# Kernel optimization log

Measured on AMD Instinct MI355X. Metric: run time of the kernel, lower is better.

## Reference

```python
import jax, jax.numpy as jnp
import numpy as np

EPS = 1e-5


def _mamba(x, in_w, conv_w, conv_b, x_w, dt_w, dt_b, A_log, D, out_w):
    # x: [B, L, d_model] -> [B, L, d_model]; mamba_ssm defaults (bias-free in/out proj)
    Bsz, L, _ = x.shape
    d_inner, d_conv = conv_w.shape
    dt_rank = dt_w.shape[1]
    N = A_log.shape[1]

    xz = x @ in_w.T                              # [B, L, 2*d_inner]
    u, z = jnp.split(xz, 2, axis=-1)

    # causal depthwise conv (torch pads both sides by d_conv-1 then slices [:L])
    uc = jnp.pad(u.transpose(0, 2, 1), ((0, 0), (0, 0), (d_conv - 1, 0)))  # [B, d, L+pad]
    uc = jax.lax.conv_general_dilated(
        uc, conv_w[:, None, :], window_strides=(1,), padding='VALID',
        feature_group_count=d_inner, dimension_numbers=('NCH', 'OIH', 'NCH'))
    u = jax.nn.silu(uc + conv_b[None, :, None]).transpose(0, 2, 1)          # [B, L, d]

    xdbc = u @ x_w.T                              # [B, L, dt_rank + 2N]
    dt, Bm, Cm = jnp.split(xdbc, [dt_rank, dt_rank + N], axis=-1)
    delta = jax.nn.softplus(dt @ dt_w.T + dt_b)   # [B, L, d]

    A = -jnp.exp(A_log)                           # [d, N]
    dA = jnp.exp(delta[..., None] * A)            # [B, L, d, N]
    dBu = delta[..., None] * Bm[:, :, None, :] * u[..., None]  # [B, L, d, N]

    def step(h, inp):
        dA_t, dBu_t, C_t = inp
        h = dA_t * h + dBu_t                      # [B, d, N]
        y = jnp.einsum('bdn,bn->bd', h, C_t)
        return h, y

    h0 = jnp.zeros((Bsz, d_inner, N), dA.dtype)
    _, ys = jax.lax.scan(step, h0,
                         (dA.transpose(1, 0, 2, 3), dBu.transpose(1, 0, 2, 3), Cm.transpose(1, 0, 2)))
    y = ys.transpose(1, 0, 2)                     # [B, L, d]
    y = (y + u * D) * jax.nn.silu(z)
    return y @ out_w.T


def reference(x, input_lengths, m, emb, conv_w, conv_b, ln_g, ln_b,
              f_in_w, f_conv_w, f_conv_b, f_x_w, f_dt_w, f_dt_b, f_A_log, f_D, f_out_w,
              b_in_w, b_conv_w, b_conv_b, b_x_w, b_dt_w, b_dt_b, b_A_log, b_D, b_out_w,
              proj_w, proj_b):
    K = conv_w.shape[-1]
    pad = (K - 1) // 2
    h = emb[x].transpose(0, 2, 1)                 # [B, C, L]
    for i in range(conv_w.shape[0]):
        h = jax.lax.conv_general_dilated(h, conv_w[i], (1,), [(pad, pad)],
                                         dimension_numbers=('NCH', 'OIH', 'NCH'))
        h = h + conv_b[i][None, :, None]
        mu = h.mean(axis=1, keepdims=True)
        var = ((h - mu) ** 2).mean(axis=1, keepdims=True)
        h = (h - mu) * jax.lax.rsqrt(var + EPS)
        h = h * ln_g[i][None, :, None] + ln_b[i][None, :, None]
        h = jnp.where(h > 0, h, 0.2 * h)          # LeakyReLU(0.2); dropout is eval no-op
        h = jnp.where(m[:, None, :], 0.0, h)
    h = h.transpose(0, 2, 1)                      # [B, L, C]
    fo = _mamba(h, f_in_w, f_conv_w, f_conv_b, f_x_w, f_dt_w, f_dt_b, f_A_log, f_D, f_out_w)
    bo = _mamba(h[:, ::-1], b_in_w, b_conv_w, b_conv_b, b_x_w, b_dt_w, b_dt_b, b_A_log, b_D, b_out_w)
    comb = jnp.concatenate([fo, bo], axis=-1) @ proj_w.T + proj_b
    return jnp.where(m[:, :, None], 0.0, comb)


def setup_inputs() -> dict:
    key = jax.random.key(0)
    ks = iter(jax.random.split(key, 40))
    B, L, C, K, depth, V = 4, 1024, 512, 5, 3, 178
    d_inner, d_state, d_conv, dt_rank = 2 * C, 16, 4, 32
    inp = {
        'x': jax.random.randint(next(ks), (B, L), 0, V),
        'input_lengths': jax.random.randint(next(ks), (B,), 1, L + 1),
        'm': jnp.zeros((B, L), dtype=bool),
        'emb': jax.random.normal(next(ks), (V, C)),
        'conv_w': jax.random.normal(next(ks), (depth, C, C, K)) * 0.05,
        'conv_b': jax.random.normal(next(ks), (depth, C)) * 0.05,
        'ln_g': jnp.ones((depth, C)),
        'ln_b': jnp.zeros((depth, C)),
        'proj_w': jax.random.normal(next(ks), (C, 2 * C)) * 0.02,
        'proj_b': jax.random.normal(next(ks), (C,)) * 0.02,
    }
    for p in ('f', 'b'):
        inp[p + '_in_w'] = jax.random.normal(next(ks), (2 * d_inner, C)) * 0.02
        inp[p + '_conv_w'] = jax.random.normal(next(ks), (d_inner, d_conv)) * 0.1
        inp[p + '_conv_b'] = jax.random.normal(next(ks), (d_inner,)) * 0.1
        inp[p + '_x_w'] = jax.random.normal(next(ks), (dt_rank + 2 * d_state, d_inner)) * 0.02
        inp[p + '_dt_w'] = jax.random.normal(next(ks), (d_inner, dt_rank)) * 0.02
        inp[p + '_dt_b'] = jax.random.normal(next(ks), (d_inner,)) * 0.1
        inp[p + '_A_log'] = jax.random.uniform(next(ks), (d_inner, d_state))
        inp[p + '_D'] = jax.random.normal(next(ks), (d_inner,)) * 0.1
        inp[p + '_out_w'] = jax.random.normal(next(ks), (C, d_inner)) * 0.02
    return inp
```

## Files before the change

### kernel.cpp

```cpp
#include <hip/hip_runtime.h>
#include <hip/hip_bf16.h>

typedef __attribute__((ext_vector_type(8))) short short8;
typedef __attribute__((ext_vector_type(4))) float f32x4;
typedef __attribute__((ext_vector_type(4))) unsigned short ushort4_t;

#define BSZ 4
#define LSEQ 1024
#define CCH 512
#define BL (BSZ*LSEQ)
#define BL2 (2*BL)
#define DI 1024
#define NST 16
#define DTR 32
#define NCH 32
#define CLEN 32

__device__ __forceinline__ float sigmoidf_(float x){ return 1.f/(1.f+__expf(-x)); }
__device__ __forceinline__ float softplus_(float x){ return x > 20.f ? x : log1pf(__expf(x)); }
__device__ __forceinline__ unsigned short f2bf_(float f){
  __hip_bfloat16 h = __float2bfloat16(f); return *(unsigned short*)&h;
}

typedef const __attribute__((address_space(1))) unsigned int* gas_t;
typedef __attribute__((address_space(3))) unsigned int* las_t;
__device__ __forceinline__ void gload16(const void* g, void* l){
  __builtin_amdgcn_global_load_lds((gas_t)g, (las_t)l, 16, 0, 0);
}


struct CastEnt { const float* s; unsigned short* d; unsigned n4, acc; };
struct CastArgs { CastEnt e[9]; unsigned total4; };
__global__ void k_cast_all(CastArgs a){
  unsigned i = blockIdx.x*256 + threadIdx.x;
  if (i >= a.total4) return;
  #pragma unroll
  for (int k=0;k<9;k++){
    if (i < a.e[k].acc + a.e[k].n4){
      unsigned j = i - a.e[k].acc;
      float4 v = ((const float4*)a.e[k].s)[j];
      ushort4_t o = { f2bf_(v.x), f2bf_(v.y), f2bf_(v.z), f2bf_(v.w) };
      *(ushort4_t*)(a.e[k].d + (size_t)j*4) = o;
      return;
    }
  }
}

__global__ void k_prep_convw(const float* __restrict__ cw, __hip_bfloat16* __restrict__ wt){
  int i = blockIdx.x*256 + threadIdx.x;
  const int total = 3*CCH*CCH*5;
  if (i >= total) return;
  int j = i % (CCH*5);
  int co = (i/(CCH*5)) % CCH;
  int layer = i/(CCH*5*CCH);
  int k = j >> 9, ci = j & 511;
  wt[i] = __float2bfloat16(cw[(((size_t)layer*CCH + co)*CCH + ci)*5 + k]);
}

__global__ void k_embed(const int* __restrict__ x, const float* __restrict__ emb,
                        __hip_bfloat16* __restrict__ xpad0, __hip_bfloat16* __restrict__ xpad1){
  int i = blockIdx.x*256 + threadIdx.x;
  const int total = BSZ*(LSEQ+4)*CCH;
  const int total2 = total + BSZ*4*CCH;
  if (i >= total2) return;
  if (i >= total){
    int j = i - total;
    int c = j & (CCH-1);
    int pr = (j >> 9) & 3;
    int b = j >> 11;
    int rr = (pr < 2) ? pr : (LSEQ+2) + (pr-2);
    xpad1[((size_t)b*(LSEQ+4) + rr)*CCH + c] = __float2bfloat16(0.f);
    return;
  }
  int c = i & (CCH-1);
  int r = (i >> 9) % (LSEQ+4);
  int b = i / ((LSEQ+4)*CCH);
  float v = 0.f;
  if (r >= 2 && r < LSEQ+2){
    int tok = x[b*LSEQ + (r-2)];
    v = emb[(size_t)tok*CCH + c];
  }
  xpad0[i] = __float2bfloat16(v);
}

__global__ __launch_bounds__(256) void k_ln(
    const float* __restrict__ in, const float* __restrict__ in2,
    const float* __restrict__ g, const float* __restrict__ bb,
    const unsigned char* __restrict__ mask,
    __hip_bfloat16* __restrict__ xpad_next,
    __hip_bfloat16* __restrict__ h_enc, __hip_bfloat16* __restrict__ h_rev){
  int row = blockIdx.x;
  int b = row >> 10, l = row & 1023;
  const float* xr = in + (size_t)row*CCH;
  const float* xr2 = in2 + (size_t)row*CCH;
  int t = threadIdx.x;
  float v0 = xr[t] + xr2[t], v1 = xr[t+256] + xr2[t+256];
  float s = v0+v1, s2 = v0*v0 + v1*v1;
  #pragma unroll
  for (int off=32; off>0; off>>=1){ s += __shfl_down(s,off); s2 += __shfl_down(s2,off); }
  __shared__ float ls[8];
  if ((t&63)==0){ ls[t>>6] = s; ls[(t>>6)+4] = s2; }
  __syncthreads();
  float S  = ls[0]+ls[1]+ls[2]+ls[3];
  float S2 = ls[4]+ls[5]+ls[6]+ls[7];
  float mu = S*(1.f/CCH);
  float var = S2*(1.f/CCH) - mu*mu;
  float rs = rsqrtf(var + 1e-5f);
  bool mk = mask[row] != 0;
  #pragma unroll
  for (int e=0; e<2; e++){
    int c = t + e*256;
    float v = e ? v1 : v0;
    float h = (v-mu)*rs*g[c] + bb[c];
    h = h > 0.f ? h : 0.2f*h;
    if (mk) h = 0.f;
    __hip_bfloat16 hb = __float2bfloat16(h);
    if (xpad_next) xpad_next[((size_t)b*(LSEQ+4) + (l+2))*CCH + c] = hb;
    if (h_enc) h_enc[(size_t)row*CCH + c] = hb;
    if (h_rev) h_rev[((size_t)(b<<10) + (1023-l))*CCH + c] = hb;
  }
}

__global__ __launch_bounds__(256) void k_gemm_ksplit(
    const __hip_bfloat16* __restrict__ A, int lda,
    const __hip_bfloat16* __restrict__ W, size_t wStride,
    float* __restrict__ Cout, int ldc, int K, unsigned short* __restrict__ dtb){
  __shared__ float red[4*1024];
  int m0 = blockIdx.x << 4;
  const __hip_bfloat16* Wd = W + (size_t)(m0 >> 12)*wStride;
  int tid = threadIdx.x;
  int w = tid >> 6, lane = tid & 63;
  int r = lane & 15, kg = lane >> 4;
  int Kw = K >> 2;
  int kbase = w*Kw;

  const short* Ap = (const short*)A + (size_t)(m0 + r)*lda + kbase + kg*8;
  const short* Wp[4];
  #pragma unroll
  for (int nj=0; nj<4; nj++)
    Wp[nj] = (const short*)Wd + (size_t)(nj*16 + r)*K + kbase + kg*8;

  f32x4 acc[4];
  #pragma unroll
  for (int nj=0;nj<4;nj++) acc[nj] = (f32x4){0.f,0.f,0.f,0.f};

  for (int kk=0; kk<Kw; kk+=32){
    short8 a = *(const short8*)(Ap + kk);
    #pragma unroll
    for (int nj=0;nj<4;nj++){
      short8 wv = *(const short8*)(Wp[nj] + kk);
      acc[nj] = __builtin_amdgcn_mfma_f32_16x16x32_bf16(a, wv, acc[nj], 0,0,0);
    }
  }
  #pragma unroll
  for (int nj=0;nj<4;nj++)
    #pragma unroll
    for (int reg=0; reg<4; reg++){
      int rowt = kg*4 + reg;
      int col  = nj*16 + r;
      red[w*1024 + rowt*64 + col] = acc[nj][reg];
    }
  __syncthreads();
  int e0 = tid*4;
  f32x4 s = *(const f32x4*)&red[e0];
  #pragma unroll
  for (int ww=1; ww<4; ww++){
    f32x4 p = *(const f32x4*)&red[ww*1024 + e0];
    s.x += p.x; s.y += p.y; s.z += p.z; s.w += p.w;
  }
  int rowt = e0 >> 6, col = e0 & 63;
  *(f32x4*)&Cout[(size_t)(m0+rowt)*ldc + col] = s;
  if (col < 32){
    ushort4_t o = { f2bf_(s.x), f2bf_(s.y), f2bf_(s.z), f2bf_(s.w) };
    *(ushort4_t*)&dtb[(size_t)(m0+rowt)*32 + col] = o;
  }
}

template<bool OUTBF>
__global__ __launch_bounds__(256) void k_gemm_big(
    const __hip_bfloat16* __restrict__ A, int lda, int padExtra,
    const __hip_bfloat16* __restrict__ W, size_t wStride,
    void* __restrict__ C0, void* __restrict__ C1, int ldc, int coloff,
    int tiles_n, int baseBlocks, int totalBlocks, int Kc, int Kb,
    const float* __restrict__ bias, int biasStride, int act,
    const unsigned char* __restrict__ mask, int outRowSub, int dirColOff){
  __shared__ alignas(16) __hip_bfloat16 smem[3][6144];
  int b = blockIdx.x;
  int wg = (b & 7)*(totalBlocks >> 3) + (b >> 3);
  int seg = (wg >= baseBlocks) ? 1 : 0;
  int bid = wg - seg*baseBlocks;
  int tn = bid % tiles_n;
  int tm = bid / tiles_n;
  int m0 = tm*128, n0 = tn*64;
  int dir = m0 >> 12;
  int kOff = seg*Kc;
  const __hip_bfloat16* Wd = W + (size_t)dir*wStride;
  void* Cout = seg ? C1 : C0;
  const float* biasp = (bias && seg==0) ? bias + dir*biasStride : nullptr;

  int tid = threadIdx.x;
  int wid = tid >> 6, lane = tid & 63;
  int r = lane & 15, kg = lane >> 4;

  int sr = lane >> 2;
  int gs = (lane & 3) ^ ((sr >> 1) & 3);
  int arow0 = m0 + wid*16 + sr;
  int arow1 = arow0 + 64;
  int pa0 = arow0 + padExtra*(arow0 >> 10);
  int pa1 = arow1 + padExtra*(arow1 >> 10);
  size_t aoff0 = (size_t)pa0*lda + kOff + gs*8;
  size_t aoff1 = (size_t)pa1*lda + kOff + gs*8;
  int bcol = n0 + wid*16 + sr;
  size_t boff = (size_t)bcol*Kb + kOff + gs*8;

  int wr = wid >> 1, wc = wid & 1;
  int xs = (kg ^ ((r >> 1) & 3))*8;
  int afrag[4], bfrag[2];
  #pragma unroll
  for (int mi=0; mi<4; mi++) afrag[mi] = (wr*64 + mi*16 + r)*32 + xs;
  #pragma unroll
  for (int nj=0; nj<2; nj++) bfrag[nj] = 4096 + (wc*32 + nj*16 + r)*32 + xs;

  f32x4 acc[4][2];
  #pragma unroll
  for (int mi=0;mi<4;mi++)
    #pragma unroll
    for (int nj=0;nj<2;nj++) acc[mi][nj] = (f32x4){0.f,0.f,0.f,0.f};

  const int nt = Kc >> 5;
  auto stage = [&](int kt, int bufi){
    __hip_bfloat16* sb = &smem[bufi][0];
    int k0 = kt*32;
    gload16((const short*)A + aoff0 + k0, sb + wid*512);
    gload16((const short*)A + aoff1 + k0, sb + (wid+4)*512);
    gload16((const short*)W + (size_t)(Wd - W) + boff + k0, sb + 4096 + wid*512);
  };
  auto compute = [&](int bufi){
    const __hip_bfloat16* sb = &smem[bufi][0];
    short8 a[4], bb2[2];
    #pragma unroll
    for (int mi=0;mi<4;mi++) a[mi] = *(const short8*)&sb[afrag[mi]];
    #pragma unroll
    for (int nj=0;nj<2;nj++) bb2[nj] = *(const short8*)&sb[bfrag[nj]];
    #pragma unroll
    for (int mi=0;mi<4;mi++)
      #pragma unroll
      for (int nj=0;nj<2;nj++)
        acc[mi][nj] = __builtin_amdgcn_mfma_f32_16x16x32_bf16(a[mi], bb2[nj], acc[mi][nj], 0,0,0);
  };

  if (nt >= 3){
    stage(0, 0);
    stage(1, 1);
    int bi = 0;
    #pragma unroll 1
    for (int t=0; t<nt; t++){
      if (t+1 < nt) asm volatile("s_waitcnt vmcnt(3)" ::: "memory");
      else          asm volatile("s_waitcnt vmcnt(0)" ::: "memory");
      __builtin_amdgcn_s_barrier();
      __builtin_amdgcn_sched_barrier(0);
      if (t+2 < nt){
        int nb2 = bi + 2; if (nb2 >= 3) nb2 -= 3;
        stage(t+2, nb2);
      }
      compute(bi);
      bi = (bi+1 == 3) ? 0 : bi+1;
    }
  } else {
    for (int s=0; s<nt; s++) stage(s, s);
    asm volatile("s_waitcnt vmcnt(0)" ::: "memory");
    __builtin_amdgcn_s_barrier();
    __builtin_amdgcn_sched_barrier(0);
    for (int t=0; t<nt; t++) compute(t);
  }

  #pragma unroll
  for (int mi=0;mi<4;mi++){
    #pragma unroll
    for (int nj=0;nj<2;nj++){
      #pragma unroll
      for (int reg=0; reg<4; reg++){
        int row = m0 + wr*64 + mi*16 + kg*4 + reg;
        int col = n0 + wc*32 + nj*16 + r;
        float v = acc[mi][nj][reg];
        if (biasp) v += biasp[col];
        if (act == 1) v = softplus_(v);
        int row_out = row - dir*outRowSub;
        if (mask && mask[row_out]) v = 0.f;
        size_t o = (size_t)row_out*ldc + coloff + dir*dirColOff + col;
        if (OUTBF) ((__hip_bfloat16*)Cout)[o] = __float2bfloat16(v);
        else       ((float*)Cout)[o] = v;
      }
    }
  }
}


__global__ void k_dwconv(const float* __restrict__ xz,
                         const float* __restrict__ cw0, const float* __restrict__ cw1,
                         const float* __restrict__ cb0, const float* __restrict__ cb1,
                         float* __restrict__ u, __hip_bfloat16* __restrict__ ub){
  int i = blockIdx.x*256 + threadIdx.x;
  if (i >= BL2*DI/4) return;
  int d4 = i & (DI/4 - 1);
  int d = d4 << 2;
  int row = i >> 8;
  int dir = row >> 12;
  const float* cw = (dir ? cw1 : cw0) + d*4;
  const float* cb = (dir ? cb1 : cb0) + d;
  int l = row & 1023;
  int rb = row & ~1023;
  f32x4 cwv[4];
  #pragma unroll
  for (int j=0;j<4;j++) cwv[j] = *(const f32x4*)&cw[j*4];
  f32x4 acc = *(const f32x4*)cb;
  #pragma unroll
  for (int k=0;k<4;k++){
    int ll = l - 3 + k;
    if (ll >= 0){
      f32x4 xv = *(const f32x4*)&xz[(size_t)(rb + ll)*(2*DI) + d];
      acc.x = __fmaf_rn(cwv[0][k], xv.x, acc.x);
      acc.y = __fmaf_rn(cwv[1][k], xv.y, acc.y);
      acc.z = __fmaf_rn(cwv[2][k], xv.z, acc.z);
      acc.w = __fmaf_rn(cwv[3][k], xv.w, acc.w);
    }
  }
  f32x4 s;
  s.x = acc.x * sigmoidf_(acc.x);
  s.y = acc.y * sigmoidf_(acc.y);
  s.z = acc.z * sigmoidf_(acc.z);
  s.w = acc.w * sigmoidf_(acc.w);
  *(f32x4*)&u[(size_t)i*4] = s;
  ushort4_t o = { f2bf_(s.x), f2bf_(s.y), f2bf_(s.z), f2bf_(s.w) };
  *(ushort4_t*)((unsigned short*)ub + (size_t)i*4) = o;
}


__global__ __launch_bounds__(256) void k_scan_part(
    const float* __restrict__ Alog0, const float* __restrict__ Alog1,
    const float* __restrict__ dy, const float* __restrict__ u,
    const float* __restrict__ xdbc,
    float* __restrict__ Hp, float* __restrict__ Pp){
  __shared__ alignas(16) float Bsh[CLEN*16];
  int t = threadIdx.x;
  int dblk = blockIdx.x & 3;
  int c = (blockIdx.x >> 2) & (NCH-1);
  int b8 = blockIdx.x >> 7;
  const float* A_log = (b8 >> 2) ? Alog1 : Alog0;
  int d = dblk*256 + t;
  size_t blbase = (size_t)b8*LSEQ + (size_t)c*CLEN;
  if (t < CLEN*4){
    int l = t >> 2, q = t & 3;
    *(f32x4*)&Bsh[l*16 + q*4] = *(const f32x4*)&xdbc[(blbase+l)*64 + 32 + q*4];
  }
  float Af[16];
  #pragma unroll
  for (int n=0; n<16; n+=4){
    f32x4 a = *(const f32x4*)&A_log[(size_t)d*16 + n];
    Af[n]   = -__expf(a.x); Af[n+1] = -__expf(a.y);
    Af[n+2] = -__expf(a.z); Af[n+3] = -__expf(a.w);
  }
  float h[16], P[16];
  #pragma unroll
  for (int n=0;n<16;n++){ h[n]=0.f; P[n]=1.f; }
  __syncthreads();
  float dv = dy[blbase*DI + d];
  float uv = u[blbase*DI + d];
  for (int l=0; l<CLEN; l++){
    float dvn = 0.f, uvn = 0.f;
    if (l+1 < CLEN){
      dvn = dy[(blbase+l+1)*DI + d];
      uvn = u[(blbase+l+1)*DI + d];
    }
    float duv = dv*uv;
    #pragma unroll
    for (int n=0;n<16;n++){
      float dA = __expf(dv*Af[n]);
      h[n] = __fmaf_rn(dA, h[n], duv*Bsh[l*16+n]);
      P[n] *= dA;
    }
    dv = dvn; uv = uvn;
  }
  size_t pb = (((size_t)(b8*NCH + c))*DI + d)*16;
  #pragma unroll
  for (int n=0;n<16;n+=4){
    *(f32x4*)&Hp[pb+n] = (f32x4){h[n],h[n+1],h[n+2],h[n+3]};
    *(f32x4*)&Pp[pb+n] = (f32x4){P[n],P[n+1],P[n+2],P[n+3]};
  }
}

__global__ void k_scan_comb(float* __restrict__ Hp, float* __restrict__ Pp){
  int i = blockIdx.x*256 + threadIdx.x;
  if (i >= BL2*NST) return;
  int n = i & 15, row = i >> 4;
  int b8 = row >> 10, d = row & 1023;
  float hin = 0.f;
  #pragma unroll
  for (int c=0;c<NCH;c++){
    size_t idx = (((size_t)(b8*NCH + c))*DI + d)*16 + n;
    float P = Pp[idx], H = Hp[idx];
    Pp[idx] = hin;
    hin = __fmaf_rn(P, hin, H);
  }
}

__global__ __launch_bounds__(256) void k_scan_fin(
    const float* __restrict__ Alog0, const float* __restrict__ Alog1,
    const float* __restrict__ dy, const float* __restrict__ u,
    const float* __restrict__ xdbc,
    const float* __restrict__ Hin, const float* __restrict__ xz,
    const float* __restrict__ Dp0, const float* __restrict__ Dp1,
    __hip_bfloat16* __restrict__ yb){
  __shared__ alignas(16) float BCsh[CLEN*32];
  int t = threadIdx.x;
  int dblk = blockIdx.x & 3;
  int c = (blockIdx.x >> 2) & (NCH-1);
  int b8 = blockIdx.x >> 7;
  int dirb = b8 >> 2;
  const float* A_log = dirb ? Alog1 : Alog0;
  const float* Dp = dirb ? Dp1 : Dp0;
  int d = dblk*256 + t;
  size_t blbase = (size_t)b8*LSEQ + (size_t)c*CLEN;
  {
    int l = t >> 3, q = t & 7;
    *(f32x4*)&BCsh[l*32 + q*4] = *(const f32x4*)&xdbc[(blbase+l)*64 + 32 + q*4];
  }
  float Af[16];
  #pragma unroll
  for (int n=0; n<16; n+=4){
    f32x4 a = *(const f32x4*)&A_log[(size_t)d*16 + n];
    Af[n]   = -__expf(a.x); Af[n+1] = -__expf(a.y);
    Af[n+2] = -__expf(a.z); Af[n+3] = -__expf(a.w);
  }
  size_t pb = (((size_t)(b8*NCH + c))*DI + d)*16;
  float h[16];
  #pragma unroll
  for (int n=0;n<16;n+=4){
    f32x4 hv = *(const f32x4*)&Hin[pb+n];
    h[n]=hv.x; h[n+1]=hv.y; h[n+2]=hv.z; h[n+3]=hv.w;
  }
  float Dd = Dp[d];
  __syncthreads();
  float dv = dy[blbase*DI + d];
  float uv = u[blbase*DI + d];
  float zv = xz[blbase*(2*DI) + DI + d];
  for (int l=0; l<CLEN; l++){
    float dvn = 0.f, uvn = 0.f, zvn = 0.f;
    if (l+1 < CLEN){
      dvn = dy[(blbase+l+1)*DI + d];
      uvn = u[(blbase+l+1)*DI + d];
      zvn = xz[(blbase+l+1)*(2*DI) + DI + d];
    }
    float duv = dv*uv;
    float y = 0.f;
    #pragma unroll
    for (int n=0;n<16;n++){
      float dA = __expf(dv*Af[n]);
      h[n] = __fmaf_rn(dA, h[n], duv*BCsh[l*32+n]);
      y = __fmaf_rn(h[n], BCsh[l*32+16+n], y);
    }
    float g = zv * sigmoidf_(zv);
    float out = __fmaf_rn(uv, Dd, y) * g;
    yb[(blbase+l)*DI + d] = __float2bfloat16(out);
    dv = dvn; uv = uvn; zv = zvn;
  }
}


extern "C" void kernel_launch(void* const* d_in, const int* in_sizes, int n_in,
                              void* d_out, int out_size, void* d_ws, size_t ws_size,
                              hipStream_t stream){
  (void)in_sizes; (void)n_in; (void)out_size; (void)ws_size;
  const int*   x     = (const int*)d_in[0];
  const unsigned char* m = (const unsigned char*)d_in[2];
  const float* emb   = (const float*)d_in[3];
  const float* convw = (const float*)d_in[4];
  const float* convb = (const float*)d_in[5];
  const float* lng   = (const float*)d_in[6];
  const float* lnb   = (const float*)d_in[7];
  const float* projw = (const float*)d_in[8];
  const float* projb = (const float*)d_in[9];

  char* ws = (char*)d_ws;
  size_t off = 0;
  auto alloc = [&](size_t bytes)->char*{
    char* p = ws + off; off += (bytes + 255) & ~((size_t)255); return p;
  };
  auto wt_conv = (__hip_bfloat16*)alloc((size_t)3*CCH*CCH*5*2);
  auto w_in2  = (__hip_bfloat16*)alloc((size_t)2*2*DI*CCH*2);
  auto w_x2   = (__hip_bfloat16*)alloc((size_t)2*64*DI*2);
  auto w_dt2  = (__hip_bfloat16*)alloc((size_t)2*DI*DTR*2);
  auto w_out2 = (__hip_bfloat16*)alloc((size_t)2*CCH*DI*2);
  auto w_proj = (__hip_bfloat16*)alloc((size_t)CCH*1024*2);
  auto dtbias2= (float*)alloc((size_t)2*DI*4);
  auto xpad0  = (__hip_bfloat16*)alloc((size_t)BSZ*(LSEQ+4)*CCH*2);
  auto xpad1  = (__hip_bfloat16*)alloc((size_t)BSZ*(LSEQ+4)*CCH*2);
  auto scr    = (float*)alloc((size_t)8*NCH*DI*NST*4);
  auto h_cat  = (__hip_bfloat16*)alloc((size_t)BL2*CCH*2);
  auto xz2    = (float*)alloc((size_t)BL2*2*DI*4);
  auto u2     = (float*)alloc((size_t)BL2*DI*4);
  auto ub2    = (__hip_bfloat16*)alloc((size_t)BL2*DI*2);
  auto xdbc2  = (float*)alloc((size_t)BL2*64*4);
  auto dtb2   = (unsigned short*)alloc((size_t)BL2*DTR*2);
  auto dy2    = (float*)alloc((size_t)BL2*DI*4);
  auto yb2    = (__hip_bfloat16*)alloc((size_t)BL2*DI*2);
  auto fob    = (__hip_bfloat16*)alloc((size_t)BL*DI*2);
  auto Pp     = (float*)alloc((size_t)8*NCH*DI*NST*4);

  float* Hp = scr;

  auto nb = [](size_t n){ return (unsigned)((n + 255)/256); };

  k_prep_convw<<<dim3(nb((size_t)3*CCH*CCH*5)), dim3(256), 0, stream>>>(convw, wt_conv);
  {
    CastArgs ca;
    unsigned acc = 0;
    auto put = [&](int k, const void* s, void* d, unsigned n4){
      ca.e[k].s = (const float*)s; ca.e[k].d = (unsigned short*)d;
      ca.e[k].n4 = n4; ca.e[k].acc = acc; acc += n4;
    };
    for (int dir=0; dir<2; dir++){
      int base = 10 + 9*dir;
      put(dir*4+0, d_in[base+0], (unsigned short*)w_in2  + (size_t)dir*2*DI*CCH, (2*DI*CCH)/4);
      put(dir*4+1, d_in[base+3], (unsigned short*)w_x2   + (size_t)dir*64*DI,    (64*DI)/4);
      put(dir*4+2, d_in[base+4], (unsigned short*)w_dt2  + (size_t)dir*DI*DTR,   (DI*DTR)/4);
      put(dir*4+3, d_in[base+8], (unsigned short*)w_out2 + (size_t)dir*CCH*DI,   (CCH*DI)/4);
    }
    put(8, projw, w_proj, (CCH*1024)/4);
    ca.total4 = acc;
    k_cast_all<<<dim3(nb(acc)), dim3(256), 0, stream>>>(ca);
  }
  hipMemcpyAsync(dtbias2,      d_in[15], DI*sizeof(float), hipMemcpyDeviceToDevice, stream);
  hipMemcpyAsync(dtbias2 + DI, d_in[24], DI*sizeof(float), hipMemcpyDeviceToDevice, stream);

  auto gemm_big = [&](const void* A, int lda, int padE, const void* W, size_t wStride,
                  void* C0, void* C1, int ldc, int coloff,
                  int M, int N, int Kc, int Kb, int ksplit,
                  const float* bias, int biasStride, int act,
                  const unsigned char* msk, int outRowSub, int dirColOff, bool outbf){
    int tiles_n = N/64;
    int baseBlocks = (M/128)*tiles_n;
    int blocks = baseBlocks * (ksplit ? 2 : 1);
    if (outbf)
      k_gemm_big<true><<<dim3(blocks), dim3(256), 0, stream>>>((const __hip_bfloat16*)A, lda, padE,
          (const __hip_bfloat16*)W, wStride, C0, C1, ldc, coloff, tiles_n, baseBlocks, blocks,
          Kc, Kb, bias, biasStride, act, msk, outRowSub, dirColOff);
    else
      k_gemm_big<false><<<dim3(blocks), dim3(256), 0, stream>>>((const __hip_bfloat16*)A, lda, padE,
          (const __hip_bfloat16*)W, wStride, C0, C1, ldc, coloff, tiles_n, baseBlocks, blocks,
          Kc, Kb, bias, biasStride, act, msk, outRowSub, dirColOff);
  };

  k_embed<<<dim3(nb((size_t)BSZ*(LSEQ+4)*CCH + BSZ*4*CCH)), dim3(256), 0, stream>>>(x, emb, xpad0, xpad1);

  __hip_bfloat16* xp_in = xpad0;
  __hip_bfloat16* xp_out = xpad1;
  __hip_bfloat16* h_rev = h_cat + (size_t)BL*CCH;
  for (int layer=0; layer<3; layer++){
    const __hip_bfloat16* wt = wt_conv + (size_t)layer*CCH*CCH*5;
    gemm_big(xp_in, CCH, 4, wt, 0, scr, dy2, CCH, 0, BL, CCH, 1280, 2560, 1,
             convb + layer*CCH, 0, 0, nullptr, 0, 0, false);
    bool last = (layer==2);
    k_ln<<<dim3(BL), dim3(256), 0, stream>>>(scr, dy2, lng + layer*CCH, lnb + layer*CCH, m,
        last ? nullptr : xp_out, last ? h_cat : nullptr, last ? h_rev : nullptr);
    __hip_bfloat16* t2 = xp_in; xp_in = xp_out; xp_out = t2;
  }

  const float* Alog0 = (const float*)d_in[16];
  const float* Alog1 = (const float*)d_in[25];
  const float* Dp0   = (const float*)d_in[17];
  const float* Dp1   = (const float*)d_in[26];

  gemm_big(h_cat, CCH, 0, w_in2, (size_t)2*DI*CCH, xz2, xz2, 2*DI, 0,
           BL2, 2*DI, CCH, CCH, 0, nullptr, 0, 0, nullptr, 0, 0, false);
  k_dwconv<<<dim3(nb((size_t)BL2*DI/4)), dim3(256), 0, stream>>>(xz2,
      (const float*)d_in[11], (const float*)d_in[20],
      (const float*)d_in[12], (const float*)d_in[21], u2, ub2);
  k_gemm_ksplit<<<dim3(BL2/16), dim3(256), 0, stream>>>(ub2, DI, w_x2, (size_t)64*DI, xdbc2, 64, DI, dtb2);
  gemm_big(dtb2, DTR, 0, w_dt2, (size_t)DI*DTR, dy2, dy2, DI, 0,
           BL2, DI, DTR, DTR, 0, dtbias2, DI, 1, nullptr, 0, 0, false);
  k_scan_part<<<dim3(1024), dim3(256), 0, stream>>>(Alog0, Alog1, dy2, u2, xdbc2, Hp, Pp);
  k_scan_comb<<<dim3(nb((size_t)BL2*NST)), dim3(256), 0, stream>>>(Hp, Pp);
  k_scan_fin<<<dim3(1024), dim3(256), 0, stream>>>(Alog0, Alog1, dy2, u2, xdbc2, Pp, xz2, Dp0, Dp1, yb2);
  gemm_big(yb2, DI, 0, w_out2, (size_t)CCH*DI, fob, fob, DI, 0,
           BL2, CCH, DI, DI, 0, nullptr, 0, 0, nullptr, BL, 512, true);

  gemm_big(fob, DI, 0, w_proj, 0, d_out, d_out, CCH, 0,
           BL, CCH, DI, DI, 0, projb, 0, 0, m, 0, 0, false);
}
```

Baseline: 353.3 us.

## Prefetch scan inputs in 8-step register batches, use exp2 and closed-form chunk decay

Both chunked scan kernels now load the dt and u values (and z in the second pass) eight timesteps at a time into double-buffered registers, replacing the one-step-ahead prefetch so more memory loads are in flight behind the exp/FMA work. The log2(e) factor is folded into A once so each step calls exp2f directly. The first pass also drops the running per-step product of decays and instead computes the chunk's total decay at the end as exp2(A*sum(dt)), which removes 16 multiplies per step. The cost is higher register pressure, which may lower occupancy, and the product now comes from one exponential of a sum instead of a chain of products, so rounding differs slightly.

```diff
diff --git a/kernel.cpp b/kernel.cpp
--- a/kernel.cpp
+++ b/kernel.cpp
@@ -357,35 +357,49 @@
   #pragma unroll
   for (int n=0; n<16; n+=4){
     f32x4 a = *(const f32x4*)&A_log[(size_t)d*16 + n];
-    Af[n]   = -__expf(a.x); Af[n+1] = -__expf(a.y);
-    Af[n+2] = -__expf(a.z); Af[n+3] = -__expf(a.w);
-  }
-  float h[16], P[16];
-  #pragma unroll
-  for (int n=0;n<16;n++){ h[n]=0.f; P[n]=1.f; }
+    Af[n]   = -__expf(a.x)*1.442695041f; Af[n+1] = -__expf(a.y)*1.442695041f;
+    Af[n+2] = -__expf(a.z)*1.442695041f; Af[n+3] = -__expf(a.w)*1.442695041f;
+  }
+  float h[16];
+  #pragma unroll
+  for (int n=0;n<16;n++) h[n]=0.f;
+  float Sdv = 0.f;
+  const float* dyp = dy + blbase*DI + d;
+  const float* up  = u  + blbase*DI + d;
+  float dvb[2][8], uvb[2][8];
+  #pragma unroll
+  for (int j=0;j<8;j++){ dvb[0][j] = dyp[(size_t)j*DI]; uvb[0][j] = up[(size_t)j*DI]; }
   __syncthreads();
-  float dv = dy[blbase*DI + d];
-  float uv = u[blbase*DI + d];
-  for (int l=0; l<CLEN; l++){
-    float dvn = 0.f, uvn = 0.f;
-    if (l+1 < CLEN){
-      dvn = dy[(blbase+l+1)*DI + d];
-      uvn = u[(blbase+l+1)*DI + d];
-    }
-    float duv = dv*uv;
-    #pragma unroll
-    for (int n=0;n<16;n++){
-      float dA = __expf(dv*Af[n]);
-      h[n] = __fmaf_rn(dA, h[n], duv*Bsh[l*16+n]);
-      P[n] *= dA;
-    }
-    dv = dvn; uv = uvn;
+  #pragma unroll
+  for (int g=0; g<4; g++){
+    int cur = g & 1;
+    if (g+1 < 4){
+      int nxt = cur ^ 1;
+      #pragma unroll
+      for (int j=0;j<8;j++){
+        size_t l = (size_t)(g+1)*8 + j;
+        dvb[nxt][j] = dyp[l*DI]; uvb[nxt][j] = up[l*DI];
+      }
+    }
+    #pragma unroll
+    for (int j=0;j<8;j++){
+      int l = g*8 + j;
+      float dv = dvb[cur][j], uv = uvb[cur][j];
+      float duv = dv*uv;
+      Sdv += dv;
+      #pragma unroll
+      for (int n=0;n<16;n++){
+        float dA = exp2f(dv*Af[n]);
+        h[n] = __fmaf_rn(dA, h[n], duv*Bsh[l*16+n]);
+      }
+    }
   }
   size_t pb = (((size_t)(b8*NCH + c))*DI + d)*16;
   #pragma unroll
   for (int n=0;n<16;n+=4){
     *(f32x4*)&Hp[pb+n] = (f32x4){h[n],h[n+1],h[n+2],h[n+3]};
-    *(f32x4*)&Pp[pb+n] = (f32x4){P[n],P[n+1],P[n+2],P[n+3]};
+    *(f32x4*)&Pp[pb+n] = (f32x4){exp2f(Af[n]*Sdv), exp2f(Af[n+1]*Sdv),
+                                 exp2f(Af[n+2]*Sdv), exp2f(Af[n+3]*Sdv)};
   }
 }
 
@@ -429,8 +443,8 @@
   #pragma unroll
   for (int n=0; n<16; n+=4){
     f32x4 a = *(const f32x4*)&A_log[(size_t)d*16 + n];
-    Af[n]   = -__expf(a.x); Af[n+1] = -__expf(a.y);
-    Af[n+2] = -__expf(a.z); Af[n+3] = -__expf(a.w);
+    Af[n]   = -__expf(a.x)*1.442695041f; Af[n+1] = -__expf(a.y)*1.442695041f;
+    Af[n+2] = -__expf(a.z)*1.442695041f; Af[n+3] = -__expf(a.w)*1.442695041f;
   }
   size_t pb = (((size_t)(b8*NCH + c))*DI + d)*16;
   float h[16];
@@ -440,29 +454,46 @@
     h[n]=hv.x; h[n+1]=hv.y; h[n+2]=hv.z; h[n+3]=hv.w;
   }
   float Dd = Dp[d];
+  const float* dyp = dy + blbase*DI + d;
+  const float* up  = u  + blbase*DI + d;
+  const float* zp  = xz + blbase*(2*DI) + DI + d;
+  float dvb[2][8], uvb[2][8], zvb[2][8];
+  #pragma unroll
+  for (int j=0;j<8;j++){
+    dvb[0][j] = dyp[(size_t)j*DI];
+    uvb[0][j] = up[(size_t)j*DI];
+    zvb[0][j] = zp[(size_t)j*2*DI];
+  }
   __syncthreads();
-  float dv = dy[blbase*DI + d];
-  float uv = u[blbase*DI + d];
-  float zv = xz[blbase*(2*DI) + DI + d];
-  for (int l=0; l<CLEN; l++){
-    float dvn = 0.f, uvn = 0.f, zvn = 0.f;
-    if (l+1 < CLEN){
-      dvn = dy[(blbase+l+1)*DI + d];
-      uvn = u[(blbase+l+1)*DI + d];
-      zvn = xz[(blbase+l+1)*(2*DI) + DI + d];
-    }
-    float duv = dv*uv;
-    float y = 0.f;
-    #pragma unroll
-    for (int n=0;n<16;n++){
-      float dA = __expf(dv*Af[n]);
-      h[n] = __fmaf_rn(dA, h[n], duv*BCsh[l*32+n]);
-      y = __fmaf_rn(h[n], BCsh[l*32+16+n], y);
-    }
-    float g = zv * sigmoidf_(zv);
-    float out = __fmaf_rn(uv, Dd, y) * g;
-    yb[(blbase+l)*DI + d] = __float2bfloat16(out);
-    dv = dvn; uv = uvn; zv = zvn;
+  #pragma unroll
+  for (int g=0; g<4; g++){
+    int cur = g & 1;
+    if (g+1 < 4){
+      int nxt = cur ^ 1;
+      #pragma unroll
+      for (int j=0;j<8;j++){
+        size_t l = (size_t)(g+1)*8 + j;
+        dvb[nxt][j] = dyp[l*DI];
+        uvb[nxt][j] = up[l*DI];
+        zvb[nxt][j] = zp[l*2*DI];
+      }
+    }
+    #pragma unroll
+    for (int j=0;j<8;j++){
+      int l = g*8 + j;
+      float dv = dvb[cur][j], uv = uvb[cur][j], zv = zvb[cur][j];
+      float duv = dv*uv;
+      float y = 0.f;
+      #pragma unroll
+      for (int n=0;n<16;n++){
+        float dA = exp2f(dv*Af[n]);
+        h[n] = __fmaf_rn(dA, h[n], duv*BCsh[l*32+n]);
+        y = __fmaf_rn(h[n], BCsh[l*32+16+n], y);
+      }
+      float gg = zv * sigmoidf_(zv);
+      float out = __fmaf_rn(uv, Dd, y) * gg;
+      yb[(blbase+l)*DI + d] = __float2bfloat16(out);
+    }
   }
 }
 
```

Result: slower. 375.1 us (+6.2%).
